# Optimization experiments

Measured on AMD Instinct MI355X. Metric: run time of the kernel, lower is better.

The kernel has to match this reference:

```python
import jax, jax.numpy as jnp
import numpy as np
from jax import lax

EPS = 1e-6

def _pixel_coords(loc, H, W):
    # normalized [-1,1] xy -> continuous pixel coordinates (x in [.. W-0.5], y likewise)
    wh = jnp.array([W, H], dtype=loc.dtype)
    pos = 0.5 * (jnp.clip(loc, -1.0, 1.0) + 1.0) * wh - 0.5
    return pos[..., 0], pos[..., 1]

def token2map_agg_sparse(x, loc_orig, idx_agg, H, W):
    # scatter token features to the [H,W] map via nearest pixel of each original point,
    # normalized by per-pixel hit count (sparse-matrix formulation in the original).
    B, N, C = x.shape
    N0 = idx_agg.shape[1]
    px, py = _pixel_coords(loc_orig, H, W)
    ix = jnp.clip(jnp.round(px).astype(jnp.int32), 0, W - 1)
    iy = jnp.clip(jnp.round(py).astype(jnp.int32), 0, H - 1)
    idx_hw = (iy * W + ix + jnp.arange(B, dtype=jnp.int32)[:, None] * (H * W)).reshape(-1)
    vals = jnp.take_along_axis(x, idx_agg[..., None].astype(jnp.int32), axis=1)  # [B,N0,C]
    num = jax.ops.segment_sum(vals.reshape(B * N0, C), idx_hw, num_segments=B * H * W)
    cnt = jax.ops.segment_sum(jnp.ones((B * N0,), x.dtype), idx_hw, num_segments=B * H * W)
    fmap = num / (cnt + EPS)[:, None]
    return fmap.reshape(B, H, W, C).transpose(0, 3, 1, 2)  # NCHW

def map2token_agg_mat(fmap, loc_orig, idx_agg, agg_weight, N):
    # bilinear gather at each original point, then weighted aggregation to tokens via idx_agg
    B, C, H, W = fmap.shape
    N0 = idx_agg.shape[1]
    px, py = _pixel_coords(loc_orig, H, W)
    x0 = jnp.clip(jnp.floor(px).astype(jnp.int32), 0, W - 1)
    x1 = jnp.clip(x0 + 1, 0, W - 1)
    y0 = jnp.clip(jnp.floor(py).astype(jnp.int32), 0, H - 1)
    y1 = jnp.clip(y0 + 1, 0, H - 1)
    wx = jnp.minimum(x1.astype(px.dtype), px) - x0.astype(px.dtype)
    wy = jnp.minimum(y1.astype(py.dtype), py) - y0.astype(py.dtype)
    fm = fmap.transpose(0, 2, 3, 1).reshape(B, H * W, C)
    def gather(iy, ix):
        return jnp.take_along_axis(fm, (iy * W + ix)[..., None], axis=1)
    f = ((1 - wx) * (1 - wy))[..., None] * gather(y0, x0) \
      + (wx * (1 - wy))[..., None] * gather(y0, x1) \
      + ((1 - wx) * wy)[..., None] * gather(y1, x0) \
      + (wx * wy)[..., None] * gather(y1, x1)  # [B,N0,C]
    seg = (idx_agg.astype(jnp.int32) + jnp.arange(B, dtype=jnp.int32)[:, None] * N).reshape(-1)
    w = agg_weight.reshape(B * N0)
    wsum = jax.ops.segment_sum(w, seg, num_segments=B * N) + EPS
    wn = w / wsum[seg]
    out = jax.ops.segment_sum(f.reshape(B * N0, C) * wn[:, None], seg, num_segments=B * N)
    return out.reshape(B, N, C)

def dwconv2d(xmap, conv_w, conv_b):
    C = xmap.shape[1]
    y = lax.conv_general_dilated(xmap, conv_w, (1, 1), ((1, 1), (1, 1)),
                                 feature_group_count=C,
                                 dimension_numbers=('NCHW', 'OIHW', 'NCHW'))
    return y + conv_b[None, :, None, None]

def setup_inputs() -> dict:
    key = jax.random.key(0)
    ks = jax.random.split(key, 6)
    B, N, C, N0, H, W = 16, 1536, 768, 3072, 64, 48
    x = jax.random.normal(ks[0], (B, N, C), dtype=jnp.float32)
    loc = jax.random.uniform(ks[1], (B, N, 2), dtype=jnp.float32) * 2.0 - 1.0
    loc_orig = jax.random.uniform(ks[2], (B, N0, 2), dtype=jnp.float32) * 2.0 - 1.0
    idx_agg = jax.random.randint(ks[3], (B, N0), 0, N, dtype=jnp.int32)
    agg_weight = jax.random.uniform(ks[4], (B, N0, 1), dtype=jnp.float32)
    conv_w = jax.random.normal(ks[5], (C, 1, 3, 3), dtype=jnp.float32) * 0.1
    conv_b = jnp.zeros((C,), dtype=jnp.float32)
    return {"x": x, "loc": loc, "loc_orig": loc_orig, "idx_agg": idx_agg,
            "agg_weight": agg_weight, "H": H, "W": W,
            "conv_w": conv_w, "conv_b": conv_b}

def reference(x, loc, loc_orig, idx_agg, agg_weight, H, W, conv_w, conv_b):
    B, N, C = x.shape
    fmap = token2map_agg_sparse(x, loc_orig, idx_agg, H, W)       # [B,C,H,W]
    fmap = dwconv2d(fmap, conv_w, conv_b)                          # depthwise 3x3
    out = map2token_agg_mat(fmap, loc_orig, idx_agg, agg_weight, N)  # [B,N,C]
    return out
```

## Files before the change

kernel.cpp:

```cpp
#include <hip/hip_runtime.h>

#define B_    16
#define N_    1536
#define C_    768
#define N0_   3072
#define H_    64
#define W_    48
#define HW_   (H_ * W_)
#define NPTS  (B_ * N0_)
#define NTOK  (B_ * N_)
#define NPIX  (B_ * HW_)
#define NSCAN (NPIX + NTOK)
#define NBP   (NPIX / 256)
#define NBALL (NSCAN / 256)
#define EPS_  1e-6f
#define TY_   4
#define TX_   8
#define NTILE ((W_ / TX_) * (H_ / TY_))
#define NBCV  (B_ * NTILE)

__device__ __forceinline__ int xcd_swz(int bid, int n) {
    return (bid & 7) * (n >> 3) + (bid >> 3);
}

__global__ void k_wT(const float* __restrict__ w, float* __restrict__ wT) {
    int i = blockIdx.x * blockDim.x + threadIdx.x;
    if (i < C_ * 9) { int c = i / 9, k = i - c * 9; wT[k * C_ + c] = w[i]; }
}

__global__ void k_points(const float* __restrict__ loc_orig,
                         const int* __restrict__ idx_agg,
                         const float* __restrict__ agg_w,
                         int* __restrict__ pixkey, int4* __restrict__ ofs4,
                         float* __restrict__ wxa, float* __restrict__ wya,
                         float* __restrict__ wa,
                         int* __restrict__ cnt_pix, int* __restrict__ cnt_tok,
                         float* __restrict__ wsum) {
    int i = blockIdx.x * blockDim.x + threadIdx.x;
    if (i >= NPTS) return;
    int b = i / N0_;
    float lx = loc_orig[2 * (size_t)i];
    float ly = loc_orig[2 * (size_t)i + 1];
    lx = fminf(fmaxf(lx, -1.f), 1.f);
    ly = fminf(fmaxf(ly, -1.f), 1.f);
    float px = 0.5f * (lx + 1.f) * (float)W_ - 0.5f;
    float py = 0.5f * (ly + 1.f) * (float)H_ - 0.5f;
    int ixn = min(max((int)rintf(px), 0), W_ - 1);
    int iyn = min(max((int)rintf(py), 0), H_ - 1);
    int pk = b * HW_ + iyn * W_ + ixn;
    pixkey[i] = pk;
    int x0 = min(max((int)floorf(px), 0), W_ - 1);
    int x1 = min(x0 + 1, W_ - 1);
    int y0 = min(max((int)floorf(py), 0), H_ - 1);
    int y1 = min(y0 + 1, H_ - 1);
    wxa[i] = fminf((float)x1, px) - (float)x0;
    wya[i] = fminf((float)y1, py) - (float)y0;
    ofs4[i] = make_int4(y0 * W_ + x0, y0 * W_ + x1, y1 * W_ + x0, y1 * W_ + x1);
    float w = agg_w[i];
    wa[i] = w;
    atomicAdd(&cnt_pix[pk], 1);
    int tk = b * N_ + idx_agg[i];
    atomicAdd(&cnt_tok[tk], 1);
    atomicAdd(&wsum[tk], w);
}

__global__ __launch_bounds__(256)
void k_scanA(const int* __restrict__ cnt, int* __restrict__ pre, int* __restrict__ bsum) {
    __shared__ int sh[256];
    int b = blockIdx.x, t = threadIdx.x;
    int i = b * 256 + t;
    int v = cnt[i];
    sh[t] = v;
    __syncthreads();
    for (int d = 1; d < 256; d <<= 1) {
        int x = sh[t];
        int y = (t >= d) ? sh[t - d] : 0;
        __syncthreads();
        sh[t] = x + y;
        __syncthreads();
    }
    pre[i] = sh[t] - v;
    if (t == 255) bsum[b] = sh[255];
}

__global__ __launch_bounds__(256)
void k_scanB(const int* __restrict__ bsum, int* __restrict__ bbase,
             int* __restrict__ off_pix, int* __restrict__ off_tok) {
    __shared__ int sh[256];
    int t = threadIdx.x;
    int v = (t < NBP) ? bsum[t] : 0;
    sh[t] = v;
    __syncthreads();
    for (int d = 1; d < 256; d <<= 1) {
        int x = sh[t];
        int y = (t >= d) ? sh[t - d] : 0;
        __syncthreads();
        sh[t] = x + y;
        __syncthreads();
    }
    if (t < NBP) bbase[t] = sh[t] - v;
    __syncthreads();
    int nbt = NBALL - NBP;
    v = (t < nbt) ? bsum[NBP + t] : 0;
    sh[t] = v;
    __syncthreads();
    for (int d = 1; d < 256; d <<= 1) {
        int x = sh[t];
        int y = (t >= d) ? sh[t - d] : 0;
        __syncthreads();
        sh[t] = x + y;
        __syncthreads();
    }
    if (t < nbt) bbase[NBP + t] = sh[t] - v;
    if (t == 0) { off_pix[NPIX] = NPTS; off_tok[NTOK] = NPTS; }
}

__global__ __launch_bounds__(256)
void k_scanC(const int* __restrict__ pre, const int* __restrict__ bbase,
             int* __restrict__ off_pix, int* __restrict__ cur_pix,
             int* __restrict__ off_tok, int* __restrict__ cur_tok) {
    int b = blockIdx.x, t = threadIdx.x;
    int i = b * 256 + t;
    int val = pre[i] + bbase[b];
    if (b < NBP) { off_pix[i] = val; cur_pix[i] = val; }
    else { int j = i - NPIX; off_tok[j] = val; cur_tok[j] = val; }
}

__global__ void k_fill(const int* __restrict__ pixkey, const int* __restrict__ idx_agg,
                       const float* __restrict__ wxa, const float* __restrict__ wya,
                       const float* __restrict__ wa, const float* __restrict__ wsum,
                       int* __restrict__ cur_pix, int* __restrict__ cur_tok,
                       int* __restrict__ list_pix, int* __restrict__ list_tok,
                       float4* __restrict__ wts4) {
    int i = blockIdx.x * blockDim.x + threadIdx.x;
    if (i >= NPTS) return;
    int b = i / N0_;
    int tok = idx_agg[i];
    int tk = b * N_ + tok;
    int s1 = atomicAdd(&cur_pix[pixkey[i]], 1);
    list_pix[s1] = tk;
    int s2 = atomicAdd(&cur_tok[tk], 1);
    list_tok[s2] = i;
    float wn = wa[i] / (wsum[tk] + EPS_);
    float wx = wxa[i], wy = wya[i];
    wts4[i] = make_float4((1.f - wx) * (1.f - wy) * wn, wx * (1.f - wy) * wn,
                          (1.f - wx) * wy * wn,         wx * wy * wn);
}

template<int CC>
__global__ __launch_bounds__(CC / 4)
void k_scatter(const float4* __restrict__ x4, const int* __restrict__ off_pix,
               const int* __restrict__ list_pix, float4* __restrict__ fmap4,
               int cbase4) {
    int pk = xcd_swz(blockIdx.x, NPIX);
    int t = threadIdx.x;
    int s = off_pix[pk], e = off_pix[pk + 1];
    float4 a = make_float4(0.f, 0.f, 0.f, 0.f);
    for (int j = s; j < e; ++j) {
        int row = list_pix[j];
        float4 v = x4[(size_t)row * (C_ / 4) + cbase4 + t];
        a.x += v.x; a.y += v.y; a.z += v.z; a.w += v.w;
    }
    float sc = 1.f / ((float)(e - s) + EPS_);
    a.x *= sc; a.y *= sc; a.z *= sc; a.w *= sc;
    fmap4[(size_t)pk * (CC / 4) + t] = a;
}

template<int CC>
__global__ __launch_bounds__(CC)
void k_conv(const float* __restrict__ fmap, const float* __restrict__ wT,
            const float* __restrict__ cb, float* __restrict__ out, int cbase) {
    int logical = xcd_swz(blockIdx.x, NBCV);
    int b = logical / NTILE;
    int tile = logical % NTILE;
    int tx0 = (tile % (W_ / TX_)) * TX_;
    int ty0 = (tile / (W_ / TX_)) * TY_;
    int c = threadIdx.x;
    const float* base = fmap + (size_t)b * HW_ * CC + c;
    float v[TY_ + 2][TX_ + 2];
#pragma unroll
    for (int r = 0; r < TY_ + 2; ++r) {
        int yy = ty0 + r - 1;
        bool yok = (unsigned)yy < (unsigned)H_;
#pragma unroll
        for (int j = 0; j < TX_ + 2; ++j) {
            int xx = tx0 + j - 1;
            bool ok = yok && ((unsigned)xx < (unsigned)W_);
            v[r][j] = ok ? base[(size_t)(yy * W_ + xx) * CC] : 0.f;
        }
    }
    int cg = cbase + c;
    float k0 = wT[0 * C_ + cg], k1 = wT[1 * C_ + cg], k2 = wT[2 * C_ + cg];
    float k3 = wT[3 * C_ + cg], k4 = wT[4 * C_ + cg], k5 = wT[5 * C_ + cg];
    float k6 = wT[6 * C_ + cg], k7 = wT[7 * C_ + cg], k8 = wT[8 * C_ + cg];
    float bias = cb[cg];
    float* ob = out + (size_t)b * HW_ * CC + c;
#pragma unroll
    for (int r = 0; r < TY_; ++r) {
#pragma unroll
        for (int j = 0; j < TX_; ++j) {
            float acc = bias
                + k0 * v[r][j]     + k1 * v[r][j + 1]     + k2 * v[r][j + 2]
                + k3 * v[r + 1][j] + k4 * v[r + 1][j + 1] + k5 * v[r + 1][j + 2]
                + k6 * v[r + 2][j] + k7 * v[r + 2][j + 1] + k8 * v[r + 2][j + 2];
            ob[(size_t)((ty0 + r) * W_ + tx0 + j) * CC] = acc;
        }
    }
}

template<int CC>
__global__ __launch_bounds__(CC / 4)
void k_gather(const float4* __restrict__ conv4, const int* __restrict__ off_tok,
              const int* __restrict__ list_tok, const int4* __restrict__ ofs4,
              const float4* __restrict__ wts4, float4* __restrict__ out4,
              int cbase4) {
    int tk = xcd_swz(blockIdx.x, NTOK);
    int t = threadIdx.x;
    int b = tk / N_;
    int s = off_tok[tk], e = off_tok[tk + 1];
    const float4* bb = conv4 + (size_t)b * HW_ * (CC / 4) + t;
    float4 a = make_float4(0.f, 0.f, 0.f, 0.f);
    for (int j = s; j < e; ++j) {
        int i = list_tok[j];
        int4 o = ofs4[i];
        float4 w = wts4[i];
        float4 p0 = bb[(size_t)o.x * (CC / 4)];
        float4 p1 = bb[(size_t)o.y * (CC / 4)];
        float4 p2 = bb[(size_t)o.z * (CC / 4)];
        float4 p3 = bb[(size_t)o.w * (CC / 4)];
        a.x += w.x * p0.x + w.y * p1.x + w.z * p2.x + w.w * p3.x;
        a.y += w.x * p0.y + w.y * p1.y + w.z * p2.y + w.w * p3.y;
        a.z += w.x * p0.z + w.y * p1.z + w.z * p2.z + w.w * p3.z;
        a.w += w.x * p0.w + w.y * p1.w + w.z * p2.w + w.w * p3.w;
    }
    out4[(size_t)tk * (C_ / 4) + cbase4 + t] = a;
}

template<int CC>
static void run_chunks(const float4* x4, const int* off_pix, const int* list_pix,
                       const int* off_tok, const int* list_tok,
                       const int4* ofs4, const float4* wts4,
                       const float* wT, const float* cb,
                       float* fmap, float* convout, float* out,
                       hipStream_t stream) {
    constexpr int NCH = C_ / CC;
    for (int chunk = 0; chunk < NCH; ++chunk) {
        int cbase = chunk * CC;
        k_scatter<CC><<<NPIX, CC / 4, 0, stream>>>(
            x4, off_pix, list_pix, (float4*)fmap, cbase / 4);
        k_conv<CC><<<NBCV, CC, 0, stream>>>(fmap, wT, cb, convout, cbase);
        k_gather<CC><<<NTOK, CC / 4, 0, stream>>>(
            (const float4*)convout, off_tok, list_tok, ofs4, wts4,
            (float4*)out, cbase / 4);
    }
}

extern "C" void kernel_launch(void* const* d_in, const int* in_sizes, int n_in,
                              void* d_out, int out_size, void* d_ws, size_t ws_size,
                              hipStream_t stream) {
    const float* x        = (const float*)d_in[0];
    const float* loc_orig = (const float*)d_in[2];
    const int*   idx_agg  = (const int*)d_in[3];
    const float* agg_w    = (const float*)d_in[4];
    const float* conv_w   = (const float*)d_in[7];
    const float* conv_b   = (const float*)d_in[8];
    float* out = (float*)d_out;

    char* wsp = (char*)d_ws;
    size_t o = 0;
    auto alloc = [&](size_t bytes) -> void* {
        o = (o + 255) & ~(size_t)255;
        void* p = wsp + o;
        o += bytes;
        return p;
    };
    float*  wT       = (float*)alloc(C_ * 9 * sizeof(float));
    int*    pixkey   = (int*)alloc(NPTS * sizeof(int));
    int4*   ofs4     = (int4*)alloc(NPTS * sizeof(int4));
    float*  wxa      = (float*)alloc(NPTS * sizeof(float));
    float*  wya      = (float*)alloc(NPTS * sizeof(float));
    float*  wa       = (float*)alloc(NPTS * sizeof(float));
    float4* wts4     = (float4*)alloc(NPTS * sizeof(float4));
    int*    cnt_pix  = (int*)alloc((size_t)NSCAN * sizeof(int)
                                   + (size_t)NTOK * sizeof(float));
    int*    cnt_tok  = cnt_pix + NPIX;
    float*  wsum     = (float*)(cnt_tok + NTOK);
    int*    pre      = (int*)alloc((size_t)NSCAN * sizeof(int));
    int*    bsum     = (int*)alloc(NBALL * sizeof(int));
    int*    bbase    = (int*)alloc(NBALL * sizeof(int));
    int*    off_pix  = (int*)alloc((size_t)(NPIX + 1) * sizeof(int));
    int*    off_tok  = (int*)alloc((size_t)(NTOK + 1) * sizeof(int));
    int*    cur_pix  = (int*)alloc((size_t)NPIX * sizeof(int));
    int*    cur_tok  = (int*)alloc((size_t)NTOK * sizeof(int));
    int*    list_pix = (int*)alloc(NPTS * sizeof(int));
    int*    list_tok = (int*)alloc(NPTS * sizeof(int));

    size_t small_end = (o + 255) & ~(size_t)255;
    size_t perchan = (size_t)B_ * HW_ * 2 * sizeof(float);
    size_t avail = (ws_size > small_end + 1024) ? ws_size - small_end - 1024 : 0;
    int cc = 8;
    const int ladder[5] = {256, 128, 64, 32, 16};
    for (int k = 0; k < 5; ++k)
        if (avail >= (size_t)ladder[k] * perchan) { cc = ladder[k]; break; }

    float* fmap    = (float*)alloc((size_t)B_ * HW_ * cc * sizeof(float));
    float* convout = (float*)alloc((size_t)B_ * HW_ * cc * sizeof(float));

    hipMemsetAsync(cnt_pix, 0,
                   (size_t)NSCAN * sizeof(int) + (size_t)NTOK * sizeof(float),
                   stream);

    k_wT<<<(C_ * 9 + 255) / 256, 256, 0, stream>>>(conv_w, wT);
    k_points<<<NPTS / 256, 256, 0, stream>>>(loc_orig, idx_agg, agg_w,
                                             pixkey, ofs4, wxa, wya, wa,
                                             cnt_pix, cnt_tok, wsum);
    k_scanA<<<NBALL, 256, 0, stream>>>(cnt_pix, pre, bsum);
    k_scanB<<<1, 256, 0, stream>>>(bsum, bbase, off_pix, off_tok);
    k_scanC<<<NBALL, 256, 0, stream>>>(pre, bbase, off_pix, cur_pix, off_tok, cur_tok);
    k_fill<<<NPTS / 256, 256, 0, stream>>>(pixkey, idx_agg, wxa, wya, wa, wsum,
                                           cur_pix, cur_tok, list_pix, list_tok, wts4);

    const float4* x4 = (const float4*)x;
    switch (cc) {
        case 256: run_chunks<256>(x4, off_pix, list_pix, off_tok, list_tok, ofs4, wts4,
                                  wT, conv_b, fmap, convout, out, stream); break;
        case 128: run_chunks<128>(x4, off_pix, list_pix, off_tok, list_tok, ofs4, wts4,
                                  wT, conv_b, fmap, convout, out, stream); break;
        case  64: run_chunks< 64>(x4, off_pix, list_pix, off_tok, list_tok, ofs4, wts4,
                                  wT, conv_b, fmap, convout, out, stream); break;
        case  32: run_chunks< 32>(x4, off_pix, list_pix, off_tok, list_tok, ofs4, wts4,
                                  wT, conv_b, fmap, convout, out, stream); break;
        case  16: run_chunks< 16>(x4, off_pix, list_pix, off_tok, list_tok, ofs4, wts4,
                                  wT, conv_b, fmap, convout, out, stream); break;
        default:  run_chunks<  8>(x4, off_pix, list_pix, off_tok, list_tok, ofs4, wts4,
                                  wT, conv_b, fmap, convout, out, stream); break;
    }
}
```

Before: 293.3 us.

## Fuse depthwise conv into bilinear gather, computing conv on demand per sample

Removes the separate depthwise conv kernel and its intermediate buffer; the gather kernel now loads a 4x4 neighbourhood of the scattered map per point and applies the 3x3 conv combined with the bilinear weights in registers, with the bias folded in via the summed weights. Halving the per-channel workspace also lets a larger channel chunk fit, so fewer chunk iterations may run. The cost is far more loads and FLOPs per point (16 float4 loads and about 144 FMAs versus 4 loads before) plus branching on corner degeneracy, which trades one memory pass for extra gather traffic that relies on cache hits.

```diff
diff --git a/kernel.cpp b/kernel.cpp
--- a/kernel.cpp
+++ b/kernel.cpp
@@ -14,10 +14,6 @@
 #define NBP   (NPIX / 256)
 #define NBALL (NSCAN / 256)
 #define EPS_  1e-6f
-#define TY_   4
-#define TX_   8
-#define NTILE ((W_ / TX_) * (H_ / TY_))
-#define NBCV  (B_ * NTILE)
 
 __device__ __forceinline__ int xcd_swz(int bid, int n) {
     return (bid & 7) * (n >> 3) + (bid >> 3);
@@ -31,7 +27,7 @@
 __global__ void k_points(const float* __restrict__ loc_orig,
                          const int* __restrict__ idx_agg,
                          const float* __restrict__ agg_w,
-                         int* __restrict__ pixkey, int4* __restrict__ ofs4,
+                         int* __restrict__ pixkey, int4* __restrict__ crn4,
                          float* __restrict__ wxa, float* __restrict__ wya,
                          float* __restrict__ wa,
                          int* __restrict__ cnt_pix, int* __restrict__ cnt_tok,
@@ -55,7 +51,7 @@
     int y1 = min(y0 + 1, H_ - 1);
     wxa[i] = fminf((float)x1, px) - (float)x0;
     wya[i] = fminf((float)y1, py) - (float)y0;
-    ofs4[i] = make_int4(y0 * W_ + x0, y0 * W_ + x1, y1 * W_ + x0, y1 * W_ + x1);
+    crn4[i] = make_int4(x0, y0, x1 - x0, y1 - y0);
     float w = agg_w[i];
     wa[i] = w;
     atomicAdd(&cnt_pix[pk], 1);
@@ -166,92 +162,93 @@
     fmap4[(size_t)pk * (CC / 4) + t] = a;
 }
 
-template<int CC>
-__global__ __launch_bounds__(CC)
-void k_conv(const float* __restrict__ fmap, const float* __restrict__ wT,
-            const float* __restrict__ cb, float* __restrict__ out, int cbase) {
-    int logical = xcd_swz(blockIdx.x, NBCV);
-    int b = logical / NTILE;
-    int tile = logical % NTILE;
-    int tx0 = (tile % (W_ / TX_)) * TX_;
-    int ty0 = (tile / (W_ / TX_)) * TY_;
-    int c = threadIdx.x;
-    const float* base = fmap + (size_t)b * HW_ * CC + c;
-    float v[TY_ + 2][TX_ + 2];
-#pragma unroll
-    for (int r = 0; r < TY_ + 2; ++r) {
-        int yy = ty0 + r - 1;
-        bool yok = (unsigned)yy < (unsigned)H_;
-#pragma unroll
-        for (int j = 0; j < TX_ + 2; ++j) {
-            int xx = tx0 + j - 1;
-            bool ok = yok && ((unsigned)xx < (unsigned)W_);
-            v[r][j] = ok ? base[(size_t)(yy * W_ + xx) * CC] : 0.f;
+template<int RX, int RY>
+__device__ __forceinline__ float4 combo(const float4 (&P)[4][4], float4 w,
+                                        const float4 (&kc)[9]) {
+    float4 acc = make_float4(0.f, 0.f, 0.f, 0.f);
+#pragma unroll
+    for (int u = 0; u < 3; ++u) {
+#pragma unroll
+        for (int v = 0; v < 3; ++v) {
+            float4 pa = P[u][v];
+            float4 pb = P[u][v + RX];
+            float4 pc = P[u + RY][v];
+            float4 pd = P[u + RY][v + RX];
+            float4 k = kc[u * 3 + v];
+            float hx = w.x * pa.x + w.y * pb.x + w.z * pc.x + w.w * pd.x;
+            float hy = w.x * pa.y + w.y * pb.y + w.z * pc.y + w.w * pd.y;
+            float hz = w.x * pa.z + w.y * pb.z + w.z * pc.z + w.w * pd.z;
+            float hw = w.x * pa.w + w.y * pb.w + w.z * pc.w + w.w * pd.w;
+            acc.x += k.x * hx; acc.y += k.y * hy;
+            acc.z += k.z * hz; acc.w += k.w * hw;
         }
     }
-    int cg = cbase + c;
-    float k0 = wT[0 * C_ + cg], k1 = wT[1 * C_ + cg], k2 = wT[2 * C_ + cg];
-    float k3 = wT[3 * C_ + cg], k4 = wT[4 * C_ + cg], k5 = wT[5 * C_ + cg];
-    float k6 = wT[6 * C_ + cg], k7 = wT[7 * C_ + cg], k8 = wT[8 * C_ + cg];
-    float bias = cb[cg];
-    float* ob = out + (size_t)b * HW_ * CC + c;
-#pragma unroll
-    for (int r = 0; r < TY_; ++r) {
-#pragma unroll
-        for (int j = 0; j < TX_; ++j) {
-            float acc = bias
-                + k0 * v[r][j]     + k1 * v[r][j + 1]     + k2 * v[r][j + 2]
-                + k3 * v[r + 1][j] + k4 * v[r + 1][j + 1] + k5 * v[r + 1][j + 2]
-                + k6 * v[r + 2][j] + k7 * v[r + 2][j + 1] + k8 * v[r + 2][j + 2];
-            ob[(size_t)((ty0 + r) * W_ + tx0 + j) * CC] = acc;
-        }
-    }
+    return acc;
 }
 
 template<int CC>
 __global__ __launch_bounds__(CC / 4)
-void k_gather(const float4* __restrict__ conv4, const int* __restrict__ off_tok,
-              const int* __restrict__ list_tok, const int4* __restrict__ ofs4,
-              const float4* __restrict__ wts4, float4* __restrict__ out4,
-              int cbase4) {
+void k_gconv(const float4* __restrict__ fmap4, const int* __restrict__ off_tok,
+             const int* __restrict__ list_tok, const int4* __restrict__ crn4,
+             const float4* __restrict__ wts4, const float* __restrict__ wT,
+             const float* __restrict__ cb, float4* __restrict__ out4, int cbase) {
     int tk = xcd_swz(blockIdx.x, NTOK);
     int t = threadIdx.x;
     int b = tk / N_;
     int s = off_tok[tk], e = off_tok[tk + 1];
-    const float4* bb = conv4 + (size_t)b * HW_ * (CC / 4) + t;
-    float4 a = make_float4(0.f, 0.f, 0.f, 0.f);
+    float4 kc[9];
+#pragma unroll
+    for (int q = 0; q < 9; ++q)
+        kc[q] = ((const float4*)(wT + q * C_ + cbase))[t];
+    float4 bias4 = ((const float4*)(cb + cbase))[t];
+    const float4* fb = fmap4 + (size_t)b * HW_ * (CC / 4) + t;
+    float4 acc = make_float4(0.f, 0.f, 0.f, 0.f);
+    float wsumtok = 0.f;
     for (int j = s; j < e; ++j) {
         int i = list_tok[j];
-        int4 o = ofs4[i];
+        int4 cr = crn4[i];
         float4 w = wts4[i];
-        float4 p0 = bb[(size_t)o.x * (CC / 4)];
-        float4 p1 = bb[(size_t)o.y * (CC / 4)];
-        float4 p2 = bb[(size_t)o.z * (CC / 4)];
-        float4 p3 = bb[(size_t)o.w * (CC / 4)];
-        a.x += w.x * p0.x + w.y * p1.x + w.z * p2.x + w.w * p3.x;
-        a.y += w.x * p0.y + w.y * p1.y + w.z * p2.y + w.w * p3.y;
-        a.z += w.x * p0.z + w.y * p1.z + w.z * p2.z + w.w * p3.z;
-        a.w += w.x * p0.w + w.y * p1.w + w.z * p2.w + w.w * p3.w;
-    }
-    out4[(size_t)tk * (C_ / 4) + cbase4 + t] = a;
+        float4 P[4][4];
+#pragma unroll
+        for (int u = 0; u < 4; ++u) {
+            int yy = cr.y - 1 + u;
+            bool yok = (unsigned)yy < (unsigned)H_;
+#pragma unroll
+            for (int v = 0; v < 4; ++v) {
+                int xx = cr.x - 1 + v;
+                float4 p = make_float4(0.f, 0.f, 0.f, 0.f);
+                if (yok && ((unsigned)xx < (unsigned)W_))
+                    p = fb[(size_t)(yy * W_ + xx) * (CC / 4)];
+                P[u][v] = p;
+            }
+        }
+        float4 g;
+        if (cr.z) { g = cr.w ? combo<1, 1>(P, w, kc) : combo<1, 0>(P, w, kc); }
+        else      { g = cr.w ? combo<0, 1>(P, w, kc) : combo<0, 0>(P, w, kc); }
+        acc.x += g.x; acc.y += g.y; acc.z += g.z; acc.w += g.w;
+        wsumtok += w.x + w.y + w.z + w.w;
+    }
+    acc.x += bias4.x * wsumtok;
+    acc.y += bias4.y * wsumtok;
+    acc.z += bias4.z * wsumtok;
+    acc.w += bias4.w * wsumtok;
+    out4[(size_t)tk * (C_ / 4) + cbase / 4 + t] = acc;
 }
 
 template<int CC>
 static void run_chunks(const float4* x4, const int* off_pix, const int* list_pix,
                        const int* off_tok, const int* list_tok,
-                       const int4* ofs4, const float4* wts4,
+                       const int4* crn4, const float4* wts4,
                        const float* wT, const float* cb,
-                       float* fmap, float* convout, float* out,
-                       hipStream_t stream) {
+                       float* fmap, float* out, hipStream_t stream) {
     constexpr int NCH = C_ / CC;
     for (int chunk = 0; chunk < NCH; ++chunk) {
         int cbase = chunk * CC;
         k_scatter<CC><<<NPIX, CC / 4, 0, stream>>>(
             x4, off_pix, list_pix, (float4*)fmap, cbase / 4);
-        k_conv<CC><<<NBCV, CC, 0, stream>>>(fmap, wT, cb, convout, cbase);
-        k_gather<CC><<<NTOK, CC / 4, 0, stream>>>(
-            (const float4*)convout, off_tok, list_tok, ofs4, wts4,
-            (float4*)out, cbase / 4);
+        k_gconv<CC><<<NTOK, CC / 4, 0, stream>>>(
+            (const float4*)fmap, off_tok, list_tok, crn4, wts4, wT, cb,
+            (float4*)out, cbase);
     }
 }
 
@@ -276,7 +273,7 @@
     };
     float*  wT       = (float*)alloc(C_ * 9 * sizeof(float));
     int*    pixkey   = (int*)alloc(NPTS * sizeof(int));
-    int4*   ofs4     = (int4*)alloc(NPTS * sizeof(int4));
+    int4*   crn4     = (int4*)alloc(NPTS * sizeof(int4));
     float*  wxa      = (float*)alloc(NPTS * sizeof(float));
     float*  wya      = (float*)alloc(NPTS * sizeof(float));
     float*  wa       = (float*)alloc(NPTS * sizeof(float));
@@ -296,15 +293,14 @@
     int*    list_tok = (int*)alloc(NPTS * sizeof(int));
 
     size_t small_end = (o + 255) & ~(size_t)255;
-    size_t perchan = (size_t)B_ * HW_ * 2 * sizeof(float);
+    size_t perchan = (size_t)B_ * HW_ * sizeof(float);
     size_t avail = (ws_size > small_end + 1024) ? ws_size - small_end - 1024 : 0;
     int cc = 8;
     const int ladder[5] = {256, 128, 64, 32, 16};
     for (int k = 0; k < 5; ++k)
         if (avail >= (size_t)ladder[k] * perchan) { cc = ladder[k]; break; }
 
-    float* fmap    = (float*)alloc((size_t)B_ * HW_ * cc * sizeof(float));
-    float* convout = (float*)alloc((size_t)B_ * HW_ * cc * sizeof(float));
+    float* fmap = (float*)alloc((size_t)B_ * HW_ * cc * sizeof(float));
 
     hipMemsetAsync(cnt_pix, 0,
                    (size_t)NSCAN * sizeof(int) + (size_t)NTOK * sizeof(float),
@@ -312,7 +308,7 @@
 
     k_wT<<<(C_ * 9 + 255) / 256, 256, 0, stream>>>(conv_w, wT);
     k_points<<<NPTS / 256, 256, 0, stream>>>(loc_orig, idx_agg, agg_w,
-                                             pixkey, ofs4, wxa, wya, wa,
+                                             pixkey, crn4, wxa, wya, wa,
                                              cnt_pix, cnt_tok, wsum);
     k_scanA<<<NBALL, 256, 0, stream>>>(cnt_pix, pre, bsum);
     k_scanB<<<1, 256, 0, stream>>>(bsum, bbase, off_pix, off_tok);
@@ -322,17 +318,17 @@
 
     const float4* x4 = (const float4*)x;
     switch (cc) {
-        case 256: run_chunks<256>(x4, off_pix, list_pix, off_tok, list_tok, ofs4, wts4,
-                                  wT, conv_b, fmap, convout, out, stream); break;
-        case 128: run_chunks<128>(x4, off_pix, list_pix, off_tok, list_tok, ofs4, wts4,
-                                  wT, conv_b, fmap, convout, out, stream); break;
-        case  64: run_chunks< 64>(x4, off_pix, list_pix, off_tok, list_tok, ofs4, wts4,
-                                  wT, conv_b, fmap, convout, out, stream); break;
-        case  32: run_chunks< 32>(x4, off_pix, list_pix, off_tok, list_tok, ofs4, wts4,
-                                  wT, conv_b, fmap, convout, out, stream); break;
-        case  16: run_chunks< 16>(x4, off_pix, list_pix, off_tok, list_tok, ofs4, wts4,
-                                  wT, conv_b, fmap, convout, out, stream); break;
-        default:  run_chunks<  8>(x4, off_pix, list_pix, off_tok, list_tok, ofs4, wts4,
-                                  wT, conv_b, fmap, convout, out, stream); break;
-    }
-}
+        case 256: run_chunks<256>(x4, off_pix, list_pix, off_tok, list_tok, crn4, wts4,
+                                  wT, conv_b, fmap, out, stream); break;
+        case 128: run_chunks<128>(x4, off_pix, list_pix, off_tok, list_tok, crn4, wts4,
+                                  wT, conv_b, fmap, out, stream); break;
+        case  64: run_chunks< 64>(x4, off_pix, list_pix, off_tok, list_tok, crn4, wts4,
+                                  wT, conv_b, fmap, out, stream); break;
+        case  32: run_chunks< 32>(x4, off_pix, list_pix, off_tok, list_tok, crn4, wts4,
+                                  wT, conv_b, fmap, out, stream); break;
+        case  16: run_chunks< 16>(x4, off_pix, list_pix, off_tok, list_tok, crn4, wts4,
+                                  wT, conv_b, fmap, out, stream); break;
+        default:  run_chunks<  8>(x4, off_pix, list_pix, off_tok, list_tok, crn4, wts4,
+                                  wT, conv_b, fmap, out, stream); break;
+    }
+}
```

Result: slower. 334.2 us (+14.0%).

## Pack multiple pixels/tokens per block, presort gather data, fuse prologue kernels

Applied to the files above, without the earlier changes.

Scatter and gather kernels now run 256-thread blocks covering several pixels or tokens each, instead of one small CC/4-thread block per item. k_fill writes bilinear offsets and weights directly into token-sorted order, which removes the list_tok indirection and turns the gather's metadata reads into contiguous ones. Both loops prefetch the next index or metadata entry to hide dependent-load latency. k_wT is merged into k_points to save one launch. The costs are an extra int4 array per point and more live registers.

```diff
diff --git a/kernel.cpp b/kernel.cpp
--- a/kernel.cpp
+++ b/kernel.cpp
@@ -18,26 +18,28 @@
 #define TX_   8
 #define NTILE ((W_ / TX_) * (H_ / TY_))
 #define NBCV  (B_ * NTILE)
+#define NBPT  (NPTS / 256)
 
 __device__ __forceinline__ int xcd_swz(int bid, int n) {
     return (bid & 7) * (n >> 3) + (bid >> 3);
 }
 
-__global__ void k_wT(const float* __restrict__ w, float* __restrict__ wT) {
-    int i = blockIdx.x * blockDim.x + threadIdx.x;
-    if (i < C_ * 9) { int c = i / 9, k = i - c * 9; wT[k * C_ + c] = w[i]; }
-}
-
-__global__ void k_points(const float* __restrict__ loc_orig,
-                         const int* __restrict__ idx_agg,
-                         const float* __restrict__ agg_w,
-                         int* __restrict__ pixkey, int4* __restrict__ ofs4,
-                         float* __restrict__ wxa, float* __restrict__ wya,
-                         float* __restrict__ wa,
-                         int* __restrict__ cnt_pix, int* __restrict__ cnt_tok,
-                         float* __restrict__ wsum) {
-    int i = blockIdx.x * blockDim.x + threadIdx.x;
-    if (i >= NPTS) return;
+__global__ void k_pre(const float* __restrict__ loc_orig,
+                      const int* __restrict__ idx_agg,
+                      const float* __restrict__ agg_w,
+                      const float* __restrict__ conv_w, float* __restrict__ wT,
+                      int* __restrict__ pixkey, int4* __restrict__ ofs4,
+                      float* __restrict__ wxa, float* __restrict__ wya,
+                      float* __restrict__ wa,
+                      int* __restrict__ cnt_pix, int* __restrict__ cnt_tok,
+                      float* __restrict__ wsum) {
+    int bid = blockIdx.x;
+    if (bid >= NBPT) {
+        int i = (bid - NBPT) * 256 + threadIdx.x;
+        if (i < C_ * 9) { int c = i / 9, k = i - c * 9; wT[k * C_ + c] = conv_w[i]; }
+        return;
+    }
+    int i = bid * 256 + threadIdx.x;
     int b = i / N0_;
     float lx = loc_orig[2 * (size_t)i];
     float ly = loc_orig[2 * (size_t)i + 1];
@@ -127,11 +129,12 @@
 }
 
 __global__ void k_fill(const int* __restrict__ pixkey, const int* __restrict__ idx_agg,
+                       const int4* __restrict__ ofs4,
                        const float* __restrict__ wxa, const float* __restrict__ wya,
                        const float* __restrict__ wa, const float* __restrict__ wsum,
                        int* __restrict__ cur_pix, int* __restrict__ cur_tok,
-                       int* __restrict__ list_pix, int* __restrict__ list_tok,
-                       float4* __restrict__ wts4) {
+                       int* __restrict__ list_pix,
+                       int4* __restrict__ ofs_s, float4* __restrict__ wts_s) {
     int i = blockIdx.x * blockDim.x + threadIdx.x;
     if (i >= NPTS) return;
     int b = i / N0_;
@@ -140,30 +143,37 @@
     int s1 = atomicAdd(&cur_pix[pixkey[i]], 1);
     list_pix[s1] = tk;
     int s2 = atomicAdd(&cur_tok[tk], 1);
-    list_tok[s2] = i;
     float wn = wa[i] / (wsum[tk] + EPS_);
     float wx = wxa[i], wy = wya[i];
-    wts4[i] = make_float4((1.f - wx) * (1.f - wy) * wn, wx * (1.f - wy) * wn,
-                          (1.f - wx) * wy * wn,         wx * wy * wn);
+    ofs_s[s2] = ofs4[i];
+    wts_s[s2] = make_float4((1.f - wx) * (1.f - wy) * wn, wx * (1.f - wy) * wn,
+                            (1.f - wx) * wy * wn,         wx * wy * wn);
 }
 
 template<int CC>
-__global__ __launch_bounds__(CC / 4)
+__global__ __launch_bounds__(256)
 void k_scatter(const float4* __restrict__ x4, const int* __restrict__ off_pix,
                const int* __restrict__ list_pix, float4* __restrict__ fmap4,
                int cbase4) {
-    int pk = xcd_swz(blockIdx.x, NPIX);
-    int t = threadIdx.x;
+    constexpr int TPP = CC / 4;
+    constexpr int PPB = 256 / TPP;
+    int logical = xcd_swz(blockIdx.x, NPIX / PPB);
+    int slot = threadIdx.x / TPP;
+    int t = threadIdx.x - slot * TPP;
+    int pk = logical * PPB + slot;
     int s = off_pix[pk], e = off_pix[pk + 1];
     float4 a = make_float4(0.f, 0.f, 0.f, 0.f);
+    int row = 0;
+    if (s < e) row = list_pix[s];
     for (int j = s; j < e; ++j) {
-        int row = list_pix[j];
-        float4 v = x4[(size_t)row * (C_ / 4) + cbase4 + t];
+        int cur = row;
+        if (j + 1 < e) row = list_pix[j + 1];
+        float4 v = x4[(size_t)cur * (C_ / 4) + cbase4 + t];
         a.x += v.x; a.y += v.y; a.z += v.z; a.w += v.w;
     }
     float sc = 1.f / ((float)(e - s) + EPS_);
     a.x *= sc; a.y *= sc; a.z *= sc; a.w *= sc;
-    fmap4[(size_t)pk * (CC / 4) + t] = a;
+    fmap4[(size_t)pk * TPP + t] = a;
 }
 
 template<int CC>
@@ -209,48 +219,54 @@
 }
 
 template<int CC>
-__global__ __launch_bounds__(CC / 4)
+__global__ __launch_bounds__(256)
 void k_gather(const float4* __restrict__ conv4, const int* __restrict__ off_tok,
-              const int* __restrict__ list_tok, const int4* __restrict__ ofs4,
-              const float4* __restrict__ wts4, float4* __restrict__ out4,
-              int cbase4) {
-    int tk = xcd_swz(blockIdx.x, NTOK);
-    int t = threadIdx.x;
+              const int4* __restrict__ ofs_s, const float4* __restrict__ wts_s,
+              float4* __restrict__ out4, int cbase4) {
+    constexpr int TPT = CC / 4;
+    constexpr int TOKPB = 256 / TPT;
+    int logical = xcd_swz(blockIdx.x, NTOK / TOKPB);
+    int slot = threadIdx.x / TPT;
+    int t = threadIdx.x - slot * TPT;
+    int tk = logical * TOKPB + slot;
     int b = tk / N_;
     int s = off_tok[tk], e = off_tok[tk + 1];
-    const float4* bb = conv4 + (size_t)b * HW_ * (CC / 4) + t;
+    const float4* bb = conv4 + (size_t)b * HW_ * TPT + t;
     float4 a = make_float4(0.f, 0.f, 0.f, 0.f);
+    int4 o = make_int4(0, 0, 0, 0);
+    float4 w = make_float4(0.f, 0.f, 0.f, 0.f);
+    if (s < e) { o = ofs_s[s]; w = wts_s[s]; }
     for (int j = s; j < e; ++j) {
-        int i = list_tok[j];
-        int4 o = ofs4[i];
-        float4 w = wts4[i];
-        float4 p0 = bb[(size_t)o.x * (CC / 4)];
-        float4 p1 = bb[(size_t)o.y * (CC / 4)];
-        float4 p2 = bb[(size_t)o.z * (CC / 4)];
-        float4 p3 = bb[(size_t)o.w * (CC / 4)];
-        a.x += w.x * p0.x + w.y * p1.x + w.z * p2.x + w.w * p3.x;
-        a.y += w.x * p0.y + w.y * p1.y + w.z * p2.y + w.w * p3.y;
-        a.z += w.x * p0.z + w.y * p1.z + w.z * p2.z + w.w * p3.z;
-        a.w += w.x * p0.w + w.y * p1.w + w.z * p2.w + w.w * p3.w;
+        int4 oc = o; float4 wc = w;
+        if (j + 1 < e) { o = ofs_s[j + 1]; w = wts_s[j + 1]; }
+        float4 p0 = bb[(size_t)oc.x * TPT];
+        float4 p1 = bb[(size_t)oc.y * TPT];
+        float4 p2 = bb[(size_t)oc.z * TPT];
+        float4 p3 = bb[(size_t)oc.w * TPT];
+        a.x += wc.x * p0.x + wc.y * p1.x + wc.z * p2.x + wc.w * p3.x;
+        a.y += wc.x * p0.y + wc.y * p1.y + wc.z * p2.y + wc.w * p3.y;
+        a.z += wc.x * p0.z + wc.y * p1.z + wc.z * p2.z + wc.w * p3.z;
+        a.w += wc.x * p0.w + wc.y * p1.w + wc.z * p2.w + wc.w * p3.w;
     }
     out4[(size_t)tk * (C_ / 4) + cbase4 + t] = a;
 }
 
 template<int CC>
 static void run_chunks(const float4* x4, const int* off_pix, const int* list_pix,
-                       const int* off_tok, const int* list_tok,
-                       const int4* ofs4, const float4* wts4,
+                       const int* off_tok, const int4* ofs_s, const float4* wts_s,
                        const float* wT, const float* cb,
                        float* fmap, float* convout, float* out,
                        hipStream_t stream) {
     constexpr int NCH = C_ / CC;
+    constexpr int PPB = 256 / (CC / 4);
+    constexpr int TOKPB = 256 / (CC / 4);
     for (int chunk = 0; chunk < NCH; ++chunk) {
         int cbase = chunk * CC;
-        k_scatter<CC><<<NPIX, CC / 4, 0, stream>>>(
+        k_scatter<CC><<<NPIX / PPB, 256, 0, stream>>>(
             x4, off_pix, list_pix, (float4*)fmap, cbase / 4);
         k_conv<CC><<<NBCV, CC, 0, stream>>>(fmap, wT, cb, convout, cbase);
-        k_gather<CC><<<NTOK, CC / 4, 0, stream>>>(
-            (const float4*)convout, off_tok, list_tok, ofs4, wts4,
+        k_gather<CC><<<NTOK / TOKPB, 256, 0, stream>>>(
+            (const float4*)convout, off_tok, ofs_s, wts_s,
             (float4*)out, cbase / 4);
     }
 }
@@ -280,7 +296,8 @@
     float*  wxa      = (float*)alloc(NPTS * sizeof(float));
     float*  wya      = (float*)alloc(NPTS * sizeof(float));
     float*  wa       = (float*)alloc(NPTS * sizeof(float));
-    float4* wts4     = (float4*)alloc(NPTS * sizeof(float4));
+    int4*   ofs_s    = (int4*)alloc(NPTS * sizeof(int4));
+    float4* wts_s    = (float4*)alloc(NPTS * sizeof(float4));
     int*    cnt_pix  = (int*)alloc((size_t)NSCAN * sizeof(int)
                                    + (size_t)NTOK * sizeof(float));
     int*    cnt_tok  = cnt_pix + NPIX;
@@ -293,7 +310,6 @@
     int*    cur_pix  = (int*)alloc((size_t)NPIX * sizeof(int));
     int*    cur_tok  = (int*)alloc((size_t)NTOK * sizeof(int));
     int*    list_pix = (int*)alloc(NPTS * sizeof(int));
-    int*    list_tok = (int*)alloc(NPTS * sizeof(int));
 
     size_t small_end = (o + 255) & ~(size_t)255;
     size_t perchan = (size_t)B_ * HW_ * 2 * sizeof(float);
@@ -310,29 +326,28 @@
                    (size_t)NSCAN * sizeof(int) + (size_t)NTOK * sizeof(float),
                    stream);
 
-    k_wT<<<(C_ * 9 + 255) / 256, 256, 0, stream>>>(conv_w, wT);
-    k_points<<<NPTS / 256, 256, 0, stream>>>(loc_orig, idx_agg, agg_w,
-                                             pixkey, ofs4, wxa, wya, wa,
-                                             cnt_pix, cnt_tok, wsum);
+    k_pre<<<NBPT + (C_ * 9 + 255) / 256, 256, 0, stream>>>(
+        loc_orig, idx_agg, agg_w, conv_w, wT,
+        pixkey, ofs4, wxa, wya, wa, cnt_pix, cnt_tok, wsum);
     k_scanA<<<NBALL, 256, 0, stream>>>(cnt_pix, pre, bsum);
     k_scanB<<<1, 256, 0, stream>>>(bsum, bbase, off_pix, off_tok);
     k_scanC<<<NBALL, 256, 0, stream>>>(pre, bbase, off_pix, cur_pix, off_tok, cur_tok);
-    k_fill<<<NPTS / 256, 256, 0, stream>>>(pixkey, idx_agg, wxa, wya, wa, wsum,
-                                           cur_pix, cur_tok, list_pix, list_tok, wts4);
+    k_fill<<<NPTS / 256, 256, 0, stream>>>(pixkey, idx_agg, ofs4, wxa, wya, wa, wsum,
+                                           cur_pix, cur_tok, list_pix, ofs_s, wts_s);
 
     const float4* x4 = (const float4*)x;
     switch (cc) {
-        case 256: run_chunks<256>(x4, off_pix, list_pix, off_tok, list_tok, ofs4, wts4,
-                                  wT, conv_b, fmap, convout, out, stream); break;
-        case 128: run_chunks<128>(x4, off_pix, list_pix, off_tok, list_tok, ofs4, wts4,
-                                  wT, conv_b, fmap, convout, out, stream); break;
-        case  64: run_chunks< 64>(x4, off_pix, list_pix, off_tok, list_tok, ofs4, wts4,
-                                  wT, conv_b, fmap, convout, out, stream); break;
-        case  32: run_chunks< 32>(x4, off_pix, list_pix, off_tok, list_tok, ofs4, wts4,
-                                  wT, conv_b, fmap, convout, out, stream); break;
-        case  16: run_chunks< 16>(x4, off_pix, list_pix, off_tok, list_tok, ofs4, wts4,
-                                  wT, conv_b, fmap, convout, out, stream); break;
-        default:  run_chunks<  8>(x4, off_pix, list_pix, off_tok, list_tok, ofs4, wts4,
-                                  wT, conv_b, fmap, convout, out, stream); break;
-    }
-}
+        case 256: run_chunks<256>(x4, off_pix, list_pix, off_tok, ofs_s, wts_s,
+                                  wT, conv_b, fmap, convout, out, stream); break;
+        case 128: run_chunks<128>(x4, off_pix, list_pix, off_tok, ofs_s, wts_s,
+                                  wT, conv_b, fmap, convout, out, stream); break;
+        case  64: run_chunks< 64>(x4, off_pix, list_pix, off_tok, ofs_s, wts_s,
+                                  wT, conv_b, fmap, convout, out, stream); break;
+        case  32: run_chunks< 32>(x4, off_pix, list_pix, off_tok, ofs_s, wts_s,
+                                  wT, conv_b, fmap, convout, out, stream); break;
+        case  16: run_chunks< 16>(x4, off_pix, list_pix, off_tok, ofs_s, wts_s,
+                                  wT, conv_b, fmap, convout, out, stream); break;
+        default:  run_chunks<  8>(x4, off_pix, list_pix, off_tok, ofs_s, wts_s,
+                                  wT, conv_b, fmap, convout, out, stream); break;
+    }
+}
```

Result: slower. 310.4 us (+5.9%).

## Software-pipeline scatter/conv/gather stages across channel chunks in fused launches

Applied to the files above, without the earlier changes.

Replaces the serial per-chunk scatter→conv→gather launch sequence with a single fused kernel. Each launch runs a gather for chunk k-2, a conv for chunk k-1 and a scatter for chunk k, dispatched by block index, using four rotating 256-channel slabs. This cuts the launch count from nine to five and lets independent stages overlap on the GPU, filling idle tail time. It also merges the weight transpose into the point-preprocessing kernel and packs four pixels or tokens per 256-thread block. In exchange it needs four full slabs of workspace and keeps the old path as a fallback.

```diff
diff --git a/kernel.cpp b/kernel.cpp
--- a/kernel.cpp
+++ b/kernel.cpp
@@ -18,26 +18,28 @@
 #define TX_   8
 #define NTILE ((W_ / TX_) * (H_ / TY_))
 #define NBCV  (B_ * NTILE)
+#define NBPT  (NPTS / 256)
 
 __device__ __forceinline__ int xcd_swz(int bid, int n) {
     return (bid & 7) * (n >> 3) + (bid >> 3);
 }
 
-__global__ void k_wT(const float* __restrict__ w, float* __restrict__ wT) {
-    int i = blockIdx.x * blockDim.x + threadIdx.x;
-    if (i < C_ * 9) { int c = i / 9, k = i - c * 9; wT[k * C_ + c] = w[i]; }
-}
-
-__global__ void k_points(const float* __restrict__ loc_orig,
-                         const int* __restrict__ idx_agg,
-                         const float* __restrict__ agg_w,
-                         int* __restrict__ pixkey, int4* __restrict__ ofs4,
-                         float* __restrict__ wxa, float* __restrict__ wya,
-                         float* __restrict__ wa,
-                         int* __restrict__ cnt_pix, int* __restrict__ cnt_tok,
-                         float* __restrict__ wsum) {
-    int i = blockIdx.x * blockDim.x + threadIdx.x;
-    if (i >= NPTS) return;
+__global__ void k_pre(const float* __restrict__ loc_orig,
+                      const int* __restrict__ idx_agg,
+                      const float* __restrict__ agg_w,
+                      const float* __restrict__ conv_w, float* __restrict__ wT,
+                      int* __restrict__ pixkey, int4* __restrict__ ofs4,
+                      float* __restrict__ wxa, float* __restrict__ wya,
+                      float* __restrict__ wa,
+                      int* __restrict__ cnt_pix, int* __restrict__ cnt_tok,
+                      float* __restrict__ wsum) {
+    int bid = blockIdx.x;
+    if (bid >= NBPT) {
+        int i = (bid - NBPT) * 256 + threadIdx.x;
+        if (i < C_ * 9) { int c = i / 9, k = i - c * 9; wT[k * C_ + c] = conv_w[i]; }
+        return;
+    }
+    int i = bid * 256 + threadIdx.x;
     int b = i / N0_;
     float lx = loc_orig[2 * (size_t)i];
     float ly = loc_orig[2 * (size_t)i + 1];
@@ -148,10 +150,101 @@
 }
 
 template<int CC>
+__global__ __launch_bounds__(256)
+void k_fused(const float4* __restrict__ x4,
+             const int* __restrict__ off_pix, const int* __restrict__ list_pix,
+             const int* __restrict__ off_tok, const int* __restrict__ list_tok,
+             const int4* __restrict__ ofs4, const float4* __restrict__ wts4,
+             const float* __restrict__ wT, const float* __restrict__ cb,
+             const float* __restrict__ fm_r, float* __restrict__ cv_w,
+             float* __restrict__ fm_w, const float* __restrict__ cv_r,
+             float4* __restrict__ out4,
+             int ngath, int nconv, int cbg, int cbc, int cbs) {
+    constexpr int TPX = CC / 4;
+    int bid = blockIdx.x;
+    if (bid < ngath) {
+        int lg = xcd_swz(bid, NTOK / 4);
+        int slot = threadIdx.x >> 6;
+        int t = threadIdx.x & 63;
+        int tk = lg * 4 + slot;
+        int b = tk / N_;
+        int s = off_tok[tk], e = off_tok[tk + 1];
+        const float4* bb = (const float4*)cv_r + (size_t)b * HW_ * TPX + t;
+        float4 a = make_float4(0.f, 0.f, 0.f, 0.f);
+        for (int j = s; j < e; ++j) {
+            int i = list_tok[j];
+            int4 o = ofs4[i];
+            float4 w = wts4[i];
+            float4 p0 = bb[(size_t)o.x * TPX];
+            float4 p1 = bb[(size_t)o.y * TPX];
+            float4 p2 = bb[(size_t)o.z * TPX];
+            float4 p3 = bb[(size_t)o.w * TPX];
+            a.x += w.x * p0.x + w.y * p1.x + w.z * p2.x + w.w * p3.x;
+            a.y += w.x * p0.y + w.y * p1.y + w.z * p2.y + w.w * p3.y;
+            a.z += w.x * p0.z + w.y * p1.z + w.z * p2.z + w.w * p3.z;
+            a.w += w.x * p0.w + w.y * p1.w + w.z * p2.w + w.w * p3.w;
+        }
+        out4[(size_t)tk * (C_ / 4) + cbg / 4 + t] = a;
+    } else if (bid < ngath + nconv) {
+        int logical = xcd_swz(bid - ngath, NBCV);
+        int b = logical / NTILE;
+        int tile = logical % NTILE;
+        int tx0 = (tile % (W_ / TX_)) * TX_;
+        int ty0 = (tile / (W_ / TX_)) * TY_;
+        int c = threadIdx.x;
+        const float* base = fm_r + (size_t)b * HW_ * CC + c;
+        float v[TY_ + 2][TX_ + 2];
+#pragma unroll
+        for (int r = 0; r < TY_ + 2; ++r) {
+            int yy = ty0 + r - 1;
+            bool yok = (unsigned)yy < (unsigned)H_;
+#pragma unroll
+            for (int j = 0; j < TX_ + 2; ++j) {
+                int xx = tx0 + j - 1;
+                bool ok = yok && ((unsigned)xx < (unsigned)W_);
+                v[r][j] = ok ? base[(size_t)(yy * W_ + xx) * CC] : 0.f;
+            }
+        }
+        int cg = cbc + c;
+        float k0 = wT[0 * C_ + cg], k1 = wT[1 * C_ + cg], k2 = wT[2 * C_ + cg];
+        float k3 = wT[3 * C_ + cg], k4 = wT[4 * C_ + cg], k5 = wT[5 * C_ + cg];
+        float k6 = wT[6 * C_ + cg], k7 = wT[7 * C_ + cg], k8 = wT[8 * C_ + cg];
+        float bias = cb[cg];
+        float* ob = cv_w + (size_t)b * HW_ * CC + c;
+#pragma unroll
+        for (int r = 0; r < TY_; ++r) {
+#pragma unroll
+            for (int j = 0; j < TX_; ++j) {
+                float acc = bias
+                    + k0 * v[r][j]     + k1 * v[r][j + 1]     + k2 * v[r][j + 2]
+                    + k3 * v[r + 1][j] + k4 * v[r + 1][j + 1] + k5 * v[r + 1][j + 2]
+                    + k6 * v[r + 2][j] + k7 * v[r + 2][j + 1] + k8 * v[r + 2][j + 2];
+                ob[(size_t)((ty0 + r) * W_ + tx0 + j) * CC] = acc;
+            }
+        }
+    } else {
+        int lg = xcd_swz(bid - ngath - nconv, NPIX / 4);
+        int slot = threadIdx.x >> 6;
+        int t = threadIdx.x & 63;
+        int pk = lg * 4 + slot;
+        int s = off_pix[pk], e = off_pix[pk + 1];
+        float4 a = make_float4(0.f, 0.f, 0.f, 0.f);
+        for (int j = s; j < e; ++j) {
+            int row = list_pix[j];
+            float4 v = x4[(size_t)row * (C_ / 4) + cbs / 4 + t];
+            a.x += v.x; a.y += v.y; a.z += v.z; a.w += v.w;
+        }
+        float sc = 1.f / ((float)(e - s) + EPS_);
+        a.x *= sc; a.y *= sc; a.z *= sc; a.w *= sc;
+        ((float4*)fm_w)[(size_t)pk * TPX + t] = a;
+    }
+}
+
+template<int CC>
 __global__ __launch_bounds__(CC / 4)
-void k_scatter(const float4* __restrict__ x4, const int* __restrict__ off_pix,
-               const int* __restrict__ list_pix, float4* __restrict__ fmap4,
-               int cbase4) {
+void k_scat_s(const float4* __restrict__ x4, const int* __restrict__ off_pix,
+              const int* __restrict__ list_pix, float4* __restrict__ fmap4,
+              int cbase4) {
     int pk = xcd_swz(blockIdx.x, NPIX);
     int t = threadIdx.x;
     int s = off_pix[pk], e = off_pix[pk + 1];
@@ -168,8 +261,8 @@
 
 template<int CC>
 __global__ __launch_bounds__(CC)
-void k_conv(const float* __restrict__ fmap, const float* __restrict__ wT,
-            const float* __restrict__ cb, float* __restrict__ out, int cbase) {
+void k_conv_s(const float* __restrict__ fmap, const float* __restrict__ wT,
+              const float* __restrict__ cb, float* __restrict__ out, int cbase) {
     int logical = xcd_swz(blockIdx.x, NBCV);
     int b = logical / NTILE;
     int tile = logical % NTILE;
@@ -210,7 +303,7 @@
 
 template<int CC>
 __global__ __launch_bounds__(CC / 4)
-void k_gather(const float4* __restrict__ conv4, const int* __restrict__ off_tok,
+void k_gath_s(const float4* __restrict__ conv4, const int* __restrict__ off_tok,
               const int* __restrict__ list_tok, const int4* __restrict__ ofs4,
               const float4* __restrict__ wts4, float4* __restrict__ out4,
               int cbase4) {
@@ -246,10 +339,10 @@
     constexpr int NCH = C_ / CC;
     for (int chunk = 0; chunk < NCH; ++chunk) {
         int cbase = chunk * CC;
-        k_scatter<CC><<<NPIX, CC / 4, 0, stream>>>(
+        k_scat_s<CC><<<NPIX, CC / 4, 0, stream>>>(
             x4, off_pix, list_pix, (float4*)fmap, cbase / 4);
-        k_conv<CC><<<NBCV, CC, 0, stream>>>(fmap, wT, cb, convout, cbase);
-        k_gather<CC><<<NTOK, CC / 4, 0, stream>>>(
+        k_conv_s<CC><<<NBCV, CC, 0, stream>>>(fmap, wT, cb, convout, cbase);
+        k_gath_s<CC><<<NTOK, CC / 4, 0, stream>>>(
             (const float4*)convout, off_tok, list_tok, ofs4, wts4,
             (float4*)out, cbase / 4);
     }
@@ -296,24 +389,15 @@
     int*    list_tok = (int*)alloc(NPTS * sizeof(int));
 
     size_t small_end = (o + 255) & ~(size_t)255;
-    size_t perchan = (size_t)B_ * HW_ * 2 * sizeof(float);
+    size_t slab = (size_t)B_ * HW_ * 256 * sizeof(float);
     size_t avail = (ws_size > small_end + 1024) ? ws_size - small_end - 1024 : 0;
-    int cc = 8;
-    const int ladder[5] = {256, 128, 64, 32, 16};
-    for (int k = 0; k < 5; ++k)
-        if (avail >= (size_t)ladder[k] * perchan) { cc = ladder[k]; break; }
-
-    float* fmap    = (float*)alloc((size_t)B_ * HW_ * cc * sizeof(float));
-    float* convout = (float*)alloc((size_t)B_ * HW_ * cc * sizeof(float));
 
     hipMemsetAsync(cnt_pix, 0,
                    (size_t)NSCAN * sizeof(int) + (size_t)NTOK * sizeof(float),
                    stream);
-
-    k_wT<<<(C_ * 9 + 255) / 256, 256, 0, stream>>>(conv_w, wT);
-    k_points<<<NPTS / 256, 256, 0, stream>>>(loc_orig, idx_agg, agg_w,
-                                             pixkey, ofs4, wxa, wya, wa,
-                                             cnt_pix, cnt_tok, wsum);
+    k_pre<<<NBPT + (C_ * 9 + 255) / 256, 256, 0, stream>>>(
+        loc_orig, idx_agg, agg_w, conv_w, wT,
+        pixkey, ofs4, wxa, wya, wa, cnt_pix, cnt_tok, wsum);
     k_scanA<<<NBALL, 256, 0, stream>>>(cnt_pix, pre, bsum);
     k_scanB<<<1, 256, 0, stream>>>(bsum, bbase, off_pix, off_tok);
     k_scanC<<<NBALL, 256, 0, stream>>>(pre, bbase, off_pix, cur_pix, off_tok, cur_tok);
@@ -321,18 +405,53 @@
                                            cur_pix, cur_tok, list_pix, list_tok, wts4);
 
     const float4* x4 = (const float4*)x;
-    switch (cc) {
-        case 256: run_chunks<256>(x4, off_pix, list_pix, off_tok, list_tok, ofs4, wts4,
-                                  wT, conv_b, fmap, convout, out, stream); break;
-        case 128: run_chunks<128>(x4, off_pix, list_pix, off_tok, list_tok, ofs4, wts4,
-                                  wT, conv_b, fmap, convout, out, stream); break;
-        case  64: run_chunks< 64>(x4, off_pix, list_pix, off_tok, list_tok, ofs4, wts4,
-                                  wT, conv_b, fmap, convout, out, stream); break;
-        case  32: run_chunks< 32>(x4, off_pix, list_pix, off_tok, list_tok, ofs4, wts4,
-                                  wT, conv_b, fmap, convout, out, stream); break;
-        case  16: run_chunks< 16>(x4, off_pix, list_pix, off_tok, list_tok, ofs4, wts4,
-                                  wT, conv_b, fmap, convout, out, stream); break;
-        default:  run_chunks<  8>(x4, off_pix, list_pix, off_tok, list_tok, ofs4, wts4,
-                                  wT, conv_b, fmap, convout, out, stream); break;
-    }
-}
+
+    if (avail >= 4 * slab) {
+        float* s0 = (float*)alloc(slab);
+        float* s1 = (float*)alloc(slab);
+        float* s2 = (float*)alloc(slab);
+        float* s3 = (float*)alloc(slab);
+        const int NG = NTOK / 4, NC = NBCV, NS = NPIX / 4;
+        auto L = [&](int ng, int nc, int ns,
+                     const float* fmr, float* cvw, float* fmw, const float* cvr,
+                     int cbg, int cbc, int cbs) {
+            k_fused<256><<<ng + nc + ns, 256, 0, stream>>>(
+                x4, off_pix, list_pix, off_tok, list_tok, ofs4, wts4,
+                wT, conv_b, fmr, cvw, fmw, cvr, (float4*)out,
+                ng, nc, cbg, cbc, cbs);
+        };
+        L(0,  0,  NS, nullptr, nullptr, s0, nullptr,   0,   0,   0);
+        L(0,  NC, NS, s0, s2, s1, nullptr,             0,   0, 256);
+        L(NG, NC, NS, s1, s3, s0, s2,                  0, 256, 512);
+        L(NG, NC, 0,  s0, s2, nullptr, s3,           256, 512,   0);
+        L(NG, 0,  0,  nullptr, nullptr, nullptr, s2, 512,   0,   0);
+    } else {
+        size_t perchan = (size_t)B_ * HW_ * 2 * sizeof(float);
+        int cc = 8;
+        const int ladder[5] = {256, 128, 64, 32, 16};
+        for (int k = 0; k < 5; ++k)
+            if (avail >= (size_t)ladder[k] * perchan) { cc = ladder[k]; break; }
+        float* fmap    = (float*)alloc((size_t)B_ * HW_ * cc * sizeof(float));
+        float* convout = (float*)alloc((size_t)B_ * HW_ * cc * sizeof(float));
+        switch (cc) {
+            case 256: run_chunks<256>(x4, off_pix, list_pix, off_tok, list_tok,
+                                      ofs4, wts4, wT, conv_b, fmap, convout, out,
+                                      stream); break;
+            case 128: run_chunks<128>(x4, off_pix, list_pix, off_tok, list_tok,
+                                      ofs4, wts4, wT, conv_b, fmap, convout, out,
+                                      stream); break;
+            case  64: run_chunks< 64>(x4, off_pix, list_pix, off_tok, list_tok,
+                                      ofs4, wts4, wT, conv_b, fmap, convout, out,
+                                      stream); break;
+            case  32: run_chunks< 32>(x4, off_pix, list_pix, off_tok, list_tok,
+                                      ofs4, wts4, wT, conv_b, fmap, convout, out,
+                                      stream); break;
+            case  16: run_chunks< 16>(x4, off_pix, list_pix, off_tok, list_tok,
+                                      ofs4, wts4, wT, conv_b, fmap, convout, out,
+                                      stream); break;
+            default:  run_chunks<  8>(x4, off_pix, list_pix, off_tok, list_tok,
+                                      ofs4, wts4, wT, conv_b, fmap, convout, out,
+                                      stream); break;
+        }
+    }
+}
```

After: 344.3 us. 1.17x slower.
